# Kernel optimization log

Hardware: AMD Instinct MI355X
Metric: run time of the kernel (lower is better)

## Reference

```python
import jax, jax.numpy as jnp
import numpy as np
from jax import lax

NEG = jnp.float32(-1e30)  # log-domain 'zero'
BLANK = 0


def setup_inputs() -> dict:
    T, N, C, S = 512, 512, 80, 128
    k0, k1, k2, k3 = jax.random.split(jax.random.key(0), 4)
    logits = jax.random.normal(k0, (T, N, C), dtype=jnp.float32)
    log_probs = jax.nn.log_softmax(logits, axis=-1)  # CTCLoss expects log-probs
    targets = jax.random.randint(k1, (N, S), 1, C).astype(jnp.int32)  # labels in [1, C-1], blank=0 excluded
    input_lengths = jax.random.randint(k2, (N,), T // 2, T + 1).astype(jnp.int32)
    target_lengths = jax.random.randint(k3, (N,), S // 2, S + 1).astype(jnp.int32)
    return {"log_probs": log_probs, "targets": targets,
            "input_lengths": input_lengths, "target_lengths": target_lengths}


def _ctc_loss(log_probs, targets, input_lengths, target_lengths):
    # log_probs: (T, N, C) log-probabilities; targets: (N, S) labels (no blanks)
    T, N, C = log_probs.shape
    S = targets.shape[1]
    L = 2 * S + 1  # extended label length: blank-interleaved

    # extended targets: [blank, y1, blank, y2, ..., yS, blank]  -> (N, L)
    ext = jnp.zeros((N, L), jnp.int32).at[:, 1::2].set(targets)
    # skip transition (s-2 -> s) allowed only if ext[s] != ext[s-2]
    # (blank positions have ext[s]==ext[s-2]==blank, so this also forbids blank skips)
    skip_ok = jnp.pad(ext[:, 2:] != ext[:, :-2], ((0, 0), (2, 0)), constant_values=False)

    # emission log-probs on the lattice: (T, N, L)
    emit = jnp.take_along_axis(log_probs, jnp.broadcast_to(ext[None], (T, N, L)), axis=2)

    # alpha at t=0: only lattice positions 0 (blank) and 1 (first label) reachable
    alpha0 = jnp.full((N, L), NEG).at[:, 0].set(emit[0, :, 0]).at[:, 1].set(emit[0, :, 1])

    def step(alpha, xs):
        em, t = xs  # em: (N, L)
        a1 = jnp.pad(alpha[:, :-1], ((0, 0), (1, 0)), constant_values=NEG)
        a2 = jnp.where(skip_ok,
                       jnp.pad(alpha[:, :-2], ((0, 0), (2, 0)), constant_values=NEG), NEG)
        m = jnp.maximum(alpha, jnp.maximum(a1, a2))
        lse = m + jnp.log(jnp.exp(alpha - m) + jnp.exp(a1 - m) + jnp.exp(a2 - m))
        new = lse + em
        # freeze alpha for finished sequences (t >= input_length)
        alpha_new = jnp.where((t < input_lengths)[:, None], new, alpha)
        return alpha_new, None

    alpha_T, _ = lax.scan(step, alpha0, (emit[1:], jnp.arange(1, T, dtype=jnp.int32)))

    # final states: last blank (2*tl) and last label (2*tl - 1)
    i1 = (2 * target_lengths)[:, None]
    v1 = jnp.take_along_axis(alpha_T, i1, axis=1)[:, 0]
    v2 = jnp.take_along_axis(alpha_T, i1 - 1, axis=1)[:, 0]
    m = jnp.maximum(v1, v2)
    loss = -(m + jnp.log(jnp.exp(v1 - m) + jnp.exp(v2 - m)))
    # zero_infinity=True: infeasible alignments -> 0 loss
    loss = jnp.where(jnp.isfinite(loss) & (loss < 1e10), loss, 0.0)
    return loss  # (N,) reduction='none'


def reference(log_probs, targets, input_lengths, target_lengths):
    return _ctc_loss(log_probs, targets, input_lengths, target_lengths)
```

## Files before the change

### kernel.cpp

```cpp
#include <hip/hip_runtime.h>


#define NEGC  (-1.0e30f)
#define LOG2E 1.4426950408889634f
#define LN2   0.6931471805599453f

constexpr int T_ = 512;
constexpr int C_ = 80;
constexpr int S_ = 128;
constexpr int U_ = 8;
constexpr int WROW = 520;

__device__ __forceinline__ float exp2a(float x) { return __builtin_amdgcn_exp2f(x); }
__device__ __forceinline__ float log2a(float x) { return __builtin_amdgcn_logf(x); }

template <int CTRL>
__device__ __forceinline__ float dppf(float old_, float src) {
    return __int_as_float(__builtin_amdgcn_update_dpp(
        __float_as_int(old_), __float_as_int(src), CTRL, 0xF, 0xF, false));
}

__device__ __forceinline__ int wave_max_bits(float m) {
    m = fmaxf(m, dppf<0x111>(m, m));
    m = fmaxf(m, dppf<0x112>(m, m));
    m = fmaxf(m, dppf<0x114>(m, m));
    m = fmaxf(m, dppf<0x118>(m, m));
    m = fmaxf(m, dppf<0x142>(m, m));
    m = fmaxf(m, dppf<0x143>(m, m));
    return __builtin_amdgcn_readlane(__float_as_int(m), 63);
}

__device__ __forceinline__ float lse2(float x, float y) {
    float m = fmaxf(x, y);
    return m + log2a(1.0f + exp2a(-fabsf(x - y)));
}
__device__ __forceinline__ float lse3(float x, float y, float z) {
    float m = fmaxf(x, fmaxf(y, z));
    return m + log2a(exp2a(x - m) + exp2a(y - m) + exp2a(z - m));
}

__global__ __launch_bounds__(64, 1) void ctc_half(
    const float* __restrict__ lp, const int* __restrict__ tgt,
    const int* __restrict__ ilen, const int* __restrict__ tlen,
    float* __restrict__ ws, int N)
{
    const int b   = blockIdx.x;
    const int n   = b >> 1;
    const int dir = b & 1;
    const int l   = threadIdx.x;

    float* ga = ws + (size_t)n * WROW;
    float* gg = ga + 260;

    const int* tn = tgt + n * S_;
    const int ext1 = tn[2 * l];
    const int ext3 = tn[2 * l + 1];
    const int prev = (l > 0) ? tn[2 * l - 1] : 0;
    const bool skip1 = (l > 0) && (ext1 != prev);
    const bool skip3 = (ext3 != ext1);
    const bool skb3  = (l < 63) && (tn[2 * l + 2] != ext3);

    int len = ilen[n];
    len = len < 1 ? 1 : (len > T_ ? T_ : len);
    const int mid = len >> 1;

    const size_t rstride = (size_t)N * C_;
    const float* lpn = lp + (size_t)n * C_;
    const float* pB = lpn;
    const float* p1 = lpn + ext1;
    const float* p3 = lpn + ext3;

    float rb[U_], r1[U_], r3[U_];

    if (dir == 0) {
        const int last = mid - 1 > 0 ? mid - 1 : 0;
        #pragma unroll
        for (int u = 0; u < U_; ++u) {
            const int r = u + 1;
            const int rc = r < mid ? r : last;
            const size_t o = (size_t)rc * rstride;
            rb[r & 7] = pB[o]; r1[r & 7] = p1[o]; r3[r & 7] = p3[o];
        }
        float p0_ = 0.f, p1_ = 0.f, p2_ = 0.f, p3_ = 0.f, p4_ = 0.f;
        int   E = -60;
        if (l == 0) {
            p0_ = exp2a(pB[0] * LOG2E + 60.0f);
            p1_ = exp2a(p1[0] * LOG2E + 60.0f);
        }
        float PbC = exp2a(rb[1] * LOG2E);
        float P1C = exp2a(r1[1] * LOG2E);
        float P3C = exp2a(r3[1] * LOG2E);
        for (int tb = 1; tb < mid; tb += U_) {
            #pragma unroll
            for (int u = 0; u < U_; ++u) {
                const int t = tb + u;
                const int slot = (1 + u) & 7;
                const int rr = t + U_;
                const int rc = rr < mid ? rr : last;
                const size_t o = (size_t)rc * rstride;
                const float nrb = pB[o], nr1 = p1[o], nr3 = p3[o];
                const int ns = (2 + u) & 7;
                const float PbN = exp2a(rb[ns] * LOG2E);
                const float P1N = exp2a(r1[ns] * LOG2E);
                const float P3N = exp2a(r3[ns] * LOG2E);
                if (t < mid) {
                    const float sm1 = dppf<0x138>(0.0f, p3_);
                    const float i0 = p0_ + sm1;
                    const float i1 = p1_ + p0_ + (skip1 ? sm1 : 0.f);
                    const float i2 = p2_ + p1_;
                    const float i3 = p3_ + p2_ + (skip3 ? p1_ : 0.f);
                    const float i4 = p4_ + p3_;
                    p0_ = i0 * PbC; p1_ = i1 * P1C; p2_ = i2 * PbC;
                    p3_ = i3 * P3C; p4_ = i4 * PbC;
                }
                PbC = PbN; P1C = P1N; P3C = P3N;
                rb[slot] = nrb; r1[slot] = nr1; r3[slot] = nr3;
            }
            const int mi = wave_max_bits(
                fmaxf(fmaxf(fmaxf(p0_, p1_), fmaxf(p2_, p3_)), p4_));
            const int e = (mi > 0) ? (((mi >> 23) & 255) - 187) : 0;
            E += e;
            p0_ = ldexpf(p0_, -e); p1_ = ldexpf(p1_, -e); p2_ = ldexpf(p2_, -e);
            p3_ = ldexpf(p3_, -e); p4_ = ldexpf(p4_, -e);
        }
        const float fE = (float)E;
        ga[4 * l + 0] = (p0_ > 0.f) ? fmaxf(log2a(p0_) + fE, NEGC) : NEGC;
        ga[4 * l + 1] = (p1_ > 0.f) ? fmaxf(log2a(p1_) + fE, NEGC) : NEGC;
        ga[4 * l + 2] = (p2_ > 0.f) ? fmaxf(log2a(p2_) + fE, NEGC) : NEGC;
        ga[4 * l + 3] = (p3_ > 0.f) ? fmaxf(log2a(p3_) + fE, NEGC) : NEGC;
        if (l == 63) ga[256] = (p4_ > 0.f) ? fmaxf(log2a(p4_) + fE, NEGC) : NEGC;
    } else {
        const int fe = len - 1;
        #pragma unroll
        for (int u = 0; u < U_; ++u) {
            int rc = fe - 1 - u; if (rc < 0) rc = 0;
            const size_t o = (size_t)rc * rstride;
            rb[u] = pB[o]; r1[u] = p1[o]; r3[u] = p3[o];
        }
        const int tl = tlen[n];
        const int sA = 2 * tl, sB = 2 * tl - 1;
        float g0_, g1_, g2_, g3_, g4_;
        int E = -60;
        {
            const size_t o = (size_t)fe * rstride;
            const float ebi = pB[o] * LOG2E + 60.0f;
            const float e1i = p1[o] * LOG2E + 60.0f;
            const float e3i = p3[o] * LOG2E + 60.0f;
            const int s0 = 4 * l;
            g0_ = (s0     == sA)                 ? exp2a(ebi) : 0.f;
            g1_ = (s0 + 1 == sA || s0 + 1 == sB) ? exp2a(e1i) : 0.f;
            g2_ = (s0 + 2 == sA)                 ? exp2a(ebi) : 0.f;
            g3_ = (s0 + 3 == sA || s0 + 3 == sB) ? exp2a(e3i) : 0.f;
            g4_ = (l == 63 && 256 == sA)         ? exp2a(ebi) : 0.f;
        }
        float PbC = exp2a(rb[0] * LOG2E);
        float P1C = exp2a(r1[0] * LOG2E);
        float P3C = exp2a(r3[0] * LOG2E);
        for (int tb = fe - 1; tb >= mid; tb -= U_) {
            #pragma unroll
            for (int u = 0; u < U_; ++u) {
                const int t = tb - u;
                const int slot = u;
                int rc = t - U_; if (rc < 0) rc = 0;
                const size_t o = (size_t)rc * rstride;
                const float nrb = pB[o], nr1 = p1[o], nr3 = p3[o];
                const int ns = (u + 1) & 7;
                const float PbN = exp2a(rb[ns] * LOG2E);
                const float P1N = exp2a(r1[ns] * LOG2E);
                const float P3N = exp2a(r3[ns] * LOG2E);
                if (t >= mid) {
                    const float x0 = dppf<0x130>(g4_, g0_);
                    const float x1 = dppf<0x130>(0.f, g1_);
                    const float i0 = g0_ + g1_;
                    const float i1 = g1_ + g2_ + (skip3 ? g3_ : 0.f);
                    const float i2 = g2_ + g3_;
                    const float i3 = g3_ + x0 + (skb3 ? x1 : 0.f);
                    g0_ = i0 * PbC; g1_ = i1 * P1C; g2_ = i2 * PbC;
                    g3_ = i3 * P3C; g4_ = g4_ * PbC;
                }
                PbC = PbN; P1C = P1N; P3C = P3N;
                rb[slot] = nrb; r1[slot] = nr1; r3[slot] = nr3;
            }
            const int mi = wave_max_bits(
                fmaxf(fmaxf(fmaxf(g0_, g1_), fmaxf(g2_, g3_)), g4_));
            const int e = (mi > 0) ? (((mi >> 23) & 255) - 187) : 0;
            E += e;
            g0_ = ldexpf(g0_, -e); g1_ = ldexpf(g1_, -e); g2_ = ldexpf(g2_, -e);
            g3_ = ldexpf(g3_, -e); g4_ = ldexpf(g4_, -e);
        }
        const float fE = (float)E;
        gg[4 * l + 0] = (g0_ > 0.f) ? fmaxf(log2a(g0_) + fE, NEGC) : NEGC;
        gg[4 * l + 1] = (g1_ > 0.f) ? fmaxf(log2a(g1_) + fE, NEGC) : NEGC;
        gg[4 * l + 2] = (g2_ > 0.f) ? fmaxf(log2a(g2_) + fE, NEGC) : NEGC;
        gg[4 * l + 3] = (g3_ > 0.f) ? fmaxf(log2a(g3_) + fE, NEGC) : NEGC;
        if (l == 63) gg[256] = (g4_ > 0.f) ? fmaxf(log2a(g4_) + fE, NEGC) : NEGC;
    }
}

__global__ __launch_bounds__(64) void ctc_comb(
    const float* __restrict__ ws, const int* __restrict__ tgt,
    const int* __restrict__ ilen, const int* __restrict__ tlen,
    float* __restrict__ out, int N)
{
    const int n = blockIdx.x;
    const int l = threadIdx.x;
    const float* ga = ws + (size_t)n * WROW;
    const float* gg = ga + 260;

    int len = ilen[n];
    len = len < 1 ? 1 : (len > T_ ? T_ : len);
    const int tl = tlen[n];

    if (len == 1) {
        if (l == 0) {
            const float v1 = ga[2 * tl];
            const float v2 = (2 * tl >= 1) ? ga[2 * tl - 1] : NEGC;
            float loss = -lse2(v1, v2) * LN2;
            if (!(loss < 1e10f) || !isfinite(loss)) loss = 0.0f;
            out[n] = loss;
        }
        return;
    }

    const int* tn = tgt + n * S_;
    const int ext1 = tn[2 * l];
    const int ext3 = tn[2 * l + 1];
    const int prev = (l > 0) ? tn[2 * l - 1] : 0;
    const bool skip1 = (l > 0) && (ext1 != prev);
    const bool skip3 = (ext3 != ext1);

    const int s0 = 4 * l;
    const float Am1 = (l > 0) ? ga[s0 - 1] : NEGC;
    const float A0 = ga[s0], A1 = ga[s0 + 1], A2 = ga[s0 + 2], A3 = ga[s0 + 3];
    const float v0 = lse2(A0, Am1)                    + gg[s0];
    const float v1 = lse3(A1, A0, skip1 ? Am1 : NEGC) + gg[s0 + 1];
    const float v2 = lse2(A2, A1)                     + gg[s0 + 2];
    const float v3 = lse3(A3, A2, skip3 ? A1 : NEGC)  + gg[s0 + 3];
    const float v4 = (l == 63) ? (lse2(ga[256], A3) + gg[256]) : NEGC;

    float m = fmaxf(fmaxf(v0, v1), fmaxf(fmaxf(v2, v3), v4));
    float ssum = exp2a(v0 - m) + exp2a(v1 - m) + exp2a(v2 - m)
               + exp2a(v3 - m) + exp2a(v4 - m);
    float M = m;
    #pragma unroll
    for (int d = 1; d < 64; d <<= 1) M = fmaxf(M, __shfl_xor(M, d));
    float r = ssum * exp2a(m - M);
    #pragma unroll
    for (int d = 1; d < 64; d <<= 1) r += __shfl_xor(r, d);
    if (l == 0) {
        float loss = -LN2 * (M + log2a(r));
        if (!(loss < 1e10f) || !isfinite(loss)) loss = 0.0f;
        out[n] = loss;
    }
}

__global__ __launch_bounds__(128) void ctc_fused(
    const float* __restrict__ lp, const int* __restrict__ tgt,
    const int* __restrict__ ilen, const int* __restrict__ tlen,
    float* __restrict__ out, int N)
{
    const int n    = blockIdx.x;
    const int wave = threadIdx.x >> 6;
    const int l    = threadIdx.x & 63;

    __shared__ float ga[2 * S_ + 1];
    __shared__ float gg[2 * S_ + 1];

    const int* tn = tgt + n * S_;
    const int ext1 = tn[2 * l];
    const int ext3 = tn[2 * l + 1];
    const int prev = (l > 0) ? tn[2 * l - 1] : 0;
    const bool skip1 = (l > 0) && (ext1 != prev);
    const bool skip3 = (ext3 != ext1);
    const bool skb1 = (tn[2 * l + 1] != tn[2 * l]);
    const bool skb3 = (l < 63) && (tn[2 * l + 2] != tn[2 * l + 1]);

    int len = ilen[n];
    len = len < 1 ? 1 : (len > T_ ? T_ : len);
    const int mid = len >> 1;

    const size_t rstride = (size_t)N * C_;
    const float* lpn = lp + (size_t)n * C_;
    const float* pB = lpn;
    const float* p1 = lpn + ext1;
    const float* p3 = lpn + ext3;

    float rb[U_], r1[U_], r3[U_];

    if (wave == 0) {
        const int last = mid - 1 > 0 ? mid - 1 : 0;
        #pragma unroll
        for (int u = 0; u < U_; ++u) {
            const int r = u + 1;
            const int rc = r < mid ? r : last;
            const size_t o = (size_t)rc * rstride;
            rb[r & 7] = pB[o]; r1[r & 7] = p1[o]; r3[r & 7] = p3[o];
        }
        float a0 = NEGC, a1 = NEGC, a2 = NEGC, a3 = NEGC, a4 = NEGC;
        {
            const float i0 = pB[0] * LOG2E;
            const float i1 = p1[0] * LOG2E;
            if (l == 0) { a0 = i0; a1 = i1; }
        }
        for (int tb = 1; tb < mid; tb += U_) {
            #pragma unroll
            for (int u = 0; u < U_; ++u) {
                const int t = tb + u;
                const int slot = (1 + u) & 7;
                const float eb = rb[slot] * LOG2E;
                const float e1 = r1[slot] * LOG2E;
                const float e3 = r3[slot] * LOG2E;
                const int rr = t + U_;
                const int rc = rr < mid ? rr : last;
                const size_t o = (size_t)rc * rstride;
                const float nrb = pB[o], nr1 = p1[o], nr3 = p3[o];
                if (t < mid) {
                    const float sm1 = dppf<0x138>(NEGC, a3);
                    const float z1 = skip1 ? sm1 : NEGC;
                    const float z3 = skip3 ? a1  : NEGC;
                    const float n0 = lse2(a0, sm1)    + eb;
                    const float n1 = lse3(a1, a0, z1) + e1;
                    const float n2 = lse2(a2, a1)     + eb;
                    const float n3 = lse3(a3, a2, z3) + e3;
                    const float n4 = lse2(a4, a3)     + eb;
                    a0 = n0; a1 = n1; a2 = n2; a3 = n3; a4 = n4;
                }
                rb[slot] = nrb; r1[slot] = nr1; r3[slot] = nr3;
            }
        }
        ga[4 * l + 0] = a0; ga[4 * l + 1] = a1;
        ga[4 * l + 2] = a2; ga[4 * l + 3] = a3;
        if (l == 63) ga[256] = a4;
    } else {
        const int fe = len - 1;
        #pragma unroll
        for (int u = 0; u < U_; ++u) {
            int rc = fe - 1 - u; if (rc < 0) rc = 0;
            const size_t o = (size_t)rc * rstride;
            rb[u] = pB[o]; r1[u] = p1[o]; r3[u] = p3[o];
        }
        const int tl = tlen[n];
        const int sA = 2 * tl, sB = 2 * tl - 1;
        float g0, g1, g2, g3, g4;
        {
            const size_t o = (size_t)fe * rstride;
            const float ebi = pB[o] * LOG2E;
            const float e1i = p1[o] * LOG2E;
            const float e3i = p3[o] * LOG2E;
            const int s0 = 4 * l;
            g0 = (s0     == sA)                 ? ebi : NEGC;
            g1 = (s0 + 1 == sA || s0 + 1 == sB) ? e1i : NEGC;
            g2 = (s0 + 2 == sA)                 ? ebi : NEGC;
            g3 = (s0 + 3 == sA || s0 + 3 == sB) ? e3i : NEGC;
            g4 = (l == 63 && 256 == sA)         ? ebi : NEGC;
        }
        for (int tb = fe - 1; tb >= mid; tb -= U_) {
            #pragma unroll
            for (int u = 0; u < U_; ++u) {
                const int t = tb - u;
                const int slot = ((fe - 1 - tb) + u) & 7;
                const float eb = rb[slot] * LOG2E;
                const float e1 = r1[slot] * LOG2E;
                const float e3 = r3[slot] * LOG2E;
                int rc = t - U_; if (rc < 0) rc = 0;
                const size_t o = (size_t)rc * rstride;
                const float nrb = pB[o], nr1 = p1[o], nr3 = p3[o];
                if (t >= mid) {
                    const float nx0 = dppf<0x130>(g4,   g0);
                    const float nx1 = dppf<0x130>(NEGC, g1);
                    const float z1 = skb1 ? g3  : NEGC;
                    const float z3 = skb3 ? nx1 : NEGC;
                    const float n0 = lse2(g0, g1)      + eb;
                    const float n1 = lse3(g1, g2, z1)  + e1;
                    const float n2 = lse2(g2, g3)      + eb;
                    const float n3 = lse3(g3, nx0, z3) + e3;
                    const float n4 = g4 + eb;
                    g0 = n0; g1 = n1; g2 = n2; g3 = n3; g4 = n4;
                }
                rb[slot] = nrb; r1[slot] = nr1; r3[slot] = nr3;
            }
        }
        gg[4 * l + 0] = g0; gg[4 * l + 1] = g1;
        gg[4 * l + 2] = g2; gg[4 * l + 3] = g3;
        if (l == 63) gg[256] = g4;
    }

    __syncthreads();

    if (wave == 0) {
        const int tl = tlen[n];
        if (len == 1) {
            if (l == 0) {
                const float v1 = ga[2 * tl];
                const float v2 = (2 * tl >= 1) ? ga[2 * tl - 1] : NEGC;
                float loss = -lse2(v1, v2) * LN2;
                if (!(loss < 1e10f) || !isfinite(loss)) loss = 0.0f;
                out[n] = loss;
            }
            return;
        }
        const int s0 = 4 * l;
        const float Am1 = (l > 0) ? ga[s0 - 1] : NEGC;
        const float A0 = ga[s0], A1 = ga[s0 + 1], A2 = ga[s0 + 2], A3 = ga[s0 + 3];
        const float v0 = lse2(A0, Am1)                    + gg[s0];
        const float v1 = lse3(A1, A0, skip1 ? Am1 : NEGC) + gg[s0 + 1];
        const float v2 = lse2(A2, A1)                     + gg[s0 + 2];
        const float v3 = lse3(A3, A2, skip3 ? A1 : NEGC)  + gg[s0 + 3];
        const float v4 = (l == 63) ? (lse2(ga[256], A3) + gg[256]) : NEGC;

        float m = fmaxf(fmaxf(v0, v1), fmaxf(fmaxf(v2, v3), v4));
        float ssum = exp2a(v0 - m) + exp2a(v1 - m) + exp2a(v2 - m)
                   + exp2a(v3 - m) + exp2a(v4 - m);
        float M = m;
        #pragma unroll
        for (int d = 1; d < 64; d <<= 1) M = fmaxf(M, __shfl_xor(M, d));
        float r = ssum * exp2a(m - M);
        #pragma unroll
        for (int d = 1; d < 64; d <<= 1) r += __shfl_xor(r, d);
        if (l == 0) {
            float loss = -LN2 * (M + log2a(r));
            if (!(loss < 1e10f) || !isfinite(loss)) loss = 0.0f;
            out[n] = loss;
        }
    }
}

extern "C" void kernel_launch(void* const* d_in, const int* in_sizes, int n_in,
                              void* d_out, int out_size, void* d_ws, size_t ws_size,
                              hipStream_t stream) {
    const float* lp  = (const float*)d_in[0];
    const int*   tg  = (const int*)  d_in[1];
    const int*   il  = (const int*)  d_in[2];
    const int*   tl  = (const int*)  d_in[3];
    float*       out = (float*)d_out;
    const int N = in_sizes[2];
    const size_t need = (size_t)N * WROW * sizeof(float);
    if (ws_size >= need) {
        ctc_half<<<2 * N, 64, 0, stream>>>(lp, tg, il, tl, (float*)d_ws, N);
        ctc_comb<<<N, 64, 0, stream>>>((const float*)d_ws, tg, il, tl, out, N);
    } else {
        ctc_fused<<<N, 128, 0, stream>>>(lp, tg, il, tl, out, N);
    }
}
```

Before: 147.9 us.

## Stage full log-prob rows in LDS with coalesced double-buffered prefetch

Each wave now loads whole 80-class rows for 8 timesteps at a time with coalesced loads (10 per lane), pre-scales them by log2e and writes them to a double-buffered shared-memory ring. The recurrence then gathers its three emissions per step from LDS instead of issuing three scattered global loads per step. Loads are issued 16 steps ahead and the loop is restructured into two 8-step halves with renormalisation between them. This trades more global bytes (full rows rather than three values) and LDS traffic for fewer uncoalesced, latency-bound gathers on the serial critical path. There is no LDS barrier, which is acceptable only because the block is a single wave.

```diff
diff --git a/kernel.cpp b/kernel.cpp
--- a/kernel.cpp
+++ b/kernel.cpp
@@ -49,6 +49,8 @@
     const int dir = b & 1;
     const int l   = threadIdx.x;
 
+    __shared__ float lds[1280];
+
     float* ga = ws + (size_t)n * WROW;
     float* gg = ga + 260;
 
@@ -64,64 +66,100 @@
     len = len < 1 ? 1 : (len > T_ ? T_ : len);
     const int mid = len >> 1;
 
-    const size_t rstride = (size_t)N * C_;
+    const int irst = N * C_;
     const float* lpn = lp + (size_t)n * C_;
-    const float* pB = lpn;
-    const float* p1 = lpn + ext1;
-    const float* p3 = lpn + ext3;
-
-    float rb[U_], r1[U_], r3[U_];
+
+    int dkr[10], ckk[10];
+    #pragma unroll
+    for (int k = 0; k < 10; ++k) {
+        const unsigned flat = (unsigned)l + 64u * k;
+        const unsigned dk = flat / 80u;
+        ckk[k] = (int)(flat - 80u * dk);
+        dkr[k] = (int)dk * irst;
+    }
+
+    float VA[10], VB[10];
+
+#define SISSUE_F(FB, V) do {                                                   \
+    const int s_ = (FB) * irst;                                                \
+    _Pragma("unroll")                                                          \
+    for (int k = 0; k < 10; ++k)                                               \
+        V[k] = lpn[(unsigned)(s_ + dkr[k] + ckk[k])];                          \
+} while (0)
+
+#define SISSUE_B(FB, V) do {                                                   \
+    const int s_ = (FB) * irst;                                                \
+    _Pragma("unroll")                                                          \
+    for (int k = 0; k < 10; ++k) {                                             \
+        int v_ = s_ - dkr[k]; v_ = v_ < 0 ? 0 : v_;                            \
+        V[k] = lpn[(unsigned)(v_ + ckk[k])];                                   \
+    }                                                                          \
+} while (0)
+
+#define SWRITE(H, V) do {                                                      \
+    _Pragma("unroll")                                                          \
+    for (int k = 0; k < 10; ++k)                                               \
+        lds[(H) * 640 + l + 64 * k] = V[k] * LOG2E;                            \
+} while (0)
+
+#define RENORM(S0, S1, S2, S3, S4) do {                                        \
+    const int mi_ = wave_max_bits(                                             \
+        fmaxf(fmaxf(fmaxf(S0, S1), fmaxf(S2, S3)), S4));                       \
+    const int e_ = (mi_ > 0) ? (((mi_ >> 23) & 255) - 187) : 0;                \
+    E += e_;                                                                   \
+    S0 = ldexpf(S0, -e_); S1 = ldexpf(S1, -e_); S2 = ldexpf(S2, -e_);          \
+    S3 = ldexpf(S3, -e_); S4 = ldexpf(S4, -e_);                                \
+} while (0)
 
     if (dir == 0) {
-        const int last = mid - 1 > 0 ? mid - 1 : 0;
-        #pragma unroll
-        for (int u = 0; u < U_; ++u) {
-            const int r = u + 1;
-            const int rc = r < mid ? r : last;
-            const size_t o = (size_t)rc * rstride;
-            rb[r & 7] = pB[o]; r1[r & 7] = p1[o]; r3[r & 7] = p3[o];
-        }
+        SISSUE_F(1, VA);  SWRITE(0, VA);
+        SISSUE_F(9, VB);  SWRITE(1, VB);
+        SISSUE_F(17, VA);
+
         float p0_ = 0.f, p1_ = 0.f, p2_ = 0.f, p3_ = 0.f, p4_ = 0.f;
         int   E = -60;
         if (l == 0) {
-            p0_ = exp2a(pB[0] * LOG2E + 60.0f);
-            p1_ = exp2a(p1[0] * LOG2E + 60.0f);
-        }
-        float PbC = exp2a(rb[1] * LOG2E);
-        float P1C = exp2a(r1[1] * LOG2E);
-        float P3C = exp2a(r3[1] * LOG2E);
-        for (int tb = 1; tb < mid; tb += U_) {
-            #pragma unroll
-            for (int u = 0; u < U_; ++u) {
-                const int t = tb + u;
-                const int slot = (1 + u) & 7;
-                const int rr = t + U_;
-                const int rc = rr < mid ? rr : last;
-                const size_t o = (size_t)rc * rstride;
-                const float nrb = pB[o], nr1 = p1[o], nr3 = p3[o];
-                const int ns = (2 + u) & 7;
-                const float PbN = exp2a(rb[ns] * LOG2E);
-                const float P1N = exp2a(r1[ns] * LOG2E);
-                const float P3N = exp2a(r3[ns] * LOG2E);
-                if (t < mid) {
-                    const float sm1 = dppf<0x138>(0.0f, p3_);
-                    const float i0 = p0_ + sm1;
-                    const float i1 = p1_ + p0_ + (skip1 ? sm1 : 0.f);
-                    const float i2 = p2_ + p1_;
-                    const float i3 = p3_ + p2_ + (skip3 ? p1_ : 0.f);
-                    const float i4 = p4_ + p3_;
-                    p0_ = i0 * PbC; p1_ = i1 * P1C; p2_ = i2 * PbC;
-                    p3_ = i3 * P3C; p4_ = i4 * PbC;
-                }
-                PbC = PbN; P1C = P1N; P3C = P3N;
-                rb[slot] = nrb; r1[slot] = nr1; r3[slot] = nr3;
-            }
-            const int mi = wave_max_bits(
-                fmaxf(fmaxf(fmaxf(p0_, p1_), fmaxf(p2_, p3_)), p4_));
-            const int e = (mi > 0) ? (((mi >> 23) & 255) - 187) : 0;
-            E += e;
-            p0_ = ldexpf(p0_, -e); p1_ = ldexpf(p1_, -e); p2_ = ldexpf(p2_, -e);
-            p3_ = ldexpf(p3_, -e); p4_ = ldexpf(p4_, -e);
+            p0_ = exp2a(lpn[0] * LOG2E + 60.0f);
+            p1_ = exp2a(lpn[ext1] * LOG2E + 60.0f);
+        }
+        float PbC = exp2a(lds[0]);
+        float P1C = exp2a(lds[ext1]);
+        float P3C = exp2a(lds[ext3]);
+        float rbN = lds[80], r1N = lds[80 + ext1], r3N = lds[80 + ext3];
+
+#define FWD_STEP(T_EXPR) do {                                                  \
+    const int t_ = (T_EXPR);                                                   \
+    const int idx2_ = t_ + 1;                        \
+    const int ofs2_ = ((idx2_ >> 3) & 1) * 640 + (idx2_ & 7) * 80;             \
+    const float rb2_ = lds[ofs2_];                                             \
+    const float r12_ = lds[ofs2_ + ext1];                                      \
+    const float r32_ = lds[ofs2_ + ext3];                                      \
+    const float PbN_ = exp2a(rbN), P1N_ = exp2a(r1N), P3N_ = exp2a(r3N);       \
+    if (t_ < mid) {                                                            \
+        const float sm1_ = dppf<0x138>(0.0f, p3_);          \
+        const float i0_ = p0_ + sm1_;                                          \
+        const float i1_ = p1_ + p0_ + (skip1 ? sm1_ : 0.f);                    \
+        const float i2_ = p2_ + p1_;                                           \
+        const float i3_ = p3_ + p2_ + (skip3 ? p1_ : 0.f);                     \
+        const float i4_ = p4_ + p3_;                                           \
+        p0_ = i0_ * PbC; p1_ = i1_ * P1C; p2_ = i2_ * PbC;                     \
+        p3_ = i3_ * P3C; p4_ = i4_ * PbC;                                      \
+    }                                                                          \
+    PbC = PbN_; P1C = P1N_; P3C = P3N_;                                        \
+    rbN = rb2_; r1N = r12_; r3N = r32_;                                        \
+} while (0)
+
+        for (int tb = 1; tb < mid; tb += 16) {
+            #pragma unroll
+            for (int u = 0; u < 8; ++u) FWD_STEP(tb + u);
+            RENORM(p0_, p1_, p2_, p3_, p4_);
+            SWRITE(0, VA);
+            SISSUE_F(tb + 24, VB);
+            #pragma unroll
+            for (int u = 8; u < 16; ++u) FWD_STEP(tb + u);
+            RENORM(p0_, p1_, p2_, p3_, p4_);
+            SWRITE(1, VB);
+            SISSUE_F(tb + 32, VA);
         }
         const float fE = (float)E;
         ga[4 * l + 0] = (p0_ > 0.f) ? fmaxf(log2a(p0_) + fE, NEGC) : NEGC;
@@ -131,21 +169,19 @@
         if (l == 63) ga[256] = (p4_ > 0.f) ? fmaxf(log2a(p4_) + fE, NEGC) : NEGC;
     } else {
         const int fe = len - 1;
-        #pragma unroll
-        for (int u = 0; u < U_; ++u) {
-            int rc = fe - 1 - u; if (rc < 0) rc = 0;
-            const size_t o = (size_t)rc * rstride;
-            rb[u] = pB[o]; r1[u] = p1[o]; r3[u] = p3[o];
-        }
+        SISSUE_B(fe - 1, VA);  SWRITE(0, VA);
+        SISSUE_B(fe - 9, VB);  SWRITE(1, VB);
+        SISSUE_B(fe - 17, VA);
+
         const int tl = tlen[n];
         const int sA = 2 * tl, sB = 2 * tl - 1;
         float g0_, g1_, g2_, g3_, g4_;
         int E = -60;
         {
-            const size_t o = (size_t)fe * rstride;
-            const float ebi = pB[o] * LOG2E + 60.0f;
-            const float e1i = p1[o] * LOG2E + 60.0f;
-            const float e3i = p3[o] * LOG2E + 60.0f;
+            const unsigned feo = (unsigned)(fe * irst);
+            const float ebi = lpn[feo] * LOG2E + 60.0f;
+            const float e1i = lpn[feo + ext1] * LOG2E + 60.0f;
+            const float e3i = lpn[feo + ext3] * LOG2E + 60.0f;
             const int s0 = 4 * l;
             g0_ = (s0     == sA)                 ? exp2a(ebi) : 0.f;
             g1_ = (s0 + 1 == sA || s0 + 1 == sB) ? exp2a(e1i) : 0.f;
@@ -153,40 +189,44 @@
             g3_ = (s0 + 3 == sA || s0 + 3 == sB) ? exp2a(e3i) : 0.f;
             g4_ = (l == 63 && 256 == sA)         ? exp2a(ebi) : 0.f;
         }
-        float PbC = exp2a(rb[0] * LOG2E);
-        float P1C = exp2a(r1[0] * LOG2E);
-        float P3C = exp2a(r3[0] * LOG2E);
-        for (int tb = fe - 1; tb >= mid; tb -= U_) {
-            #pragma unroll
-            for (int u = 0; u < U_; ++u) {
-                const int t = tb - u;
-                const int slot = u;
-                int rc = t - U_; if (rc < 0) rc = 0;
-                const size_t o = (size_t)rc * rstride;
-                const float nrb = pB[o], nr1 = p1[o], nr3 = p3[o];
-                const int ns = (u + 1) & 7;
-                const float PbN = exp2a(rb[ns] * LOG2E);
-                const float P1N = exp2a(r1[ns] * LOG2E);
-                const float P3N = exp2a(r3[ns] * LOG2E);
-                if (t >= mid) {
-                    const float x0 = dppf<0x130>(g4_, g0_);
-                    const float x1 = dppf<0x130>(0.f, g1_);
-                    const float i0 = g0_ + g1_;
-                    const float i1 = g1_ + g2_ + (skip3 ? g3_ : 0.f);
-                    const float i2 = g2_ + g3_;
-                    const float i3 = g3_ + x0 + (skb3 ? x1 : 0.f);
-                    g0_ = i0 * PbC; g1_ = i1 * P1C; g2_ = i2 * PbC;
-                    g3_ = i3 * P3C; g4_ = g4_ * PbC;
-                }
-                PbC = PbN; P1C = P1N; P3C = P3N;
-                rb[slot] = nrb; r1[slot] = nr1; r3[slot] = nr3;
-            }
-            const int mi = wave_max_bits(
-                fmaxf(fmaxf(fmaxf(g0_, g1_), fmaxf(g2_, g3_)), g4_));
-            const int e = (mi > 0) ? (((mi >> 23) & 255) - 187) : 0;
-            E += e;
-            g0_ = ldexpf(g0_, -e); g1_ = ldexpf(g1_, -e); g2_ = ldexpf(g2_, -e);
-            g3_ = ldexpf(g3_, -e); g4_ = ldexpf(g4_, -e);
+        float PbC = exp2a(lds[0]);
+        float P1C = exp2a(lds[ext1]);
+        float P3C = exp2a(lds[ext3]);
+        float rbN = lds[80], r1N = lds[80 + ext1], r3N = lds[80 + ext3];
+
+#define BWD_STEP(T_EXPR) do {                                                  \
+    const int t_ = (T_EXPR);                                                   \
+    const int idx2_ = fe + 1 - t_;                   \
+    const int ofs2_ = ((idx2_ >> 3) & 1) * 640 + (idx2_ & 7) * 80;             \
+    const float rb2_ = lds[ofs2_];                                             \
+    const float r12_ = lds[ofs2_ + ext1];                                      \
+    const float r32_ = lds[ofs2_ + ext3];                                      \
+    const float PbN_ = exp2a(rbN), P1N_ = exp2a(r1N), P3N_ = exp2a(r3N);       \
+    if (t_ >= mid) {                                                           \
+        const float x0_ = dppf<0x130>(g4_, g0_);      \
+        const float x1_ = dppf<0x130>(0.f, g1_);      \
+        const float i0_ = g0_ + g1_;                                           \
+        const float i1_ = g1_ + g2_ + (skip3 ? g3_ : 0.f);                     \
+        const float i2_ = g2_ + g3_;                                           \
+        const float i3_ = g3_ + x0_ + (skb3 ? x1_ : 0.f);                      \
+        g0_ = i0_ * PbC; g1_ = i1_ * P1C; g2_ = i2_ * PbC;                     \
+        g3_ = i3_ * P3C; g4_ = g4_ * PbC;                                      \
+    }                                                                          \
+    PbC = PbN_; P1C = P1N_; P3C = P3N_;                                        \
+    rbN = rb2_; r1N = r12_; r3N = r32_;                                        \
+} while (0)
+
+        for (int tb = fe - 1; tb >= mid; tb -= 16) {
+            #pragma unroll
+            for (int u = 0; u < 8; ++u) BWD_STEP(tb - u);
+            RENORM(g0_, g1_, g2_, g3_, g4_);
+            SWRITE(0, VA);
+            SISSUE_B(tb - 24, VB);
+            #pragma unroll
+            for (int u = 8; u < 16; ++u) BWD_STEP(tb - u);
+            RENORM(g0_, g1_, g2_, g3_, g4_);
+            SWRITE(1, VB);
+            SISSUE_B(tb - 32, VA);
         }
         const float fE = (float)E;
         gg[4 * l + 0] = (g0_ > 0.f) ? fmaxf(log2a(g0_) + fE, NEGC) : NEGC;
@@ -195,6 +235,12 @@
         gg[4 * l + 3] = (g3_ > 0.f) ? fmaxf(log2a(g3_) + fE, NEGC) : NEGC;
         if (l == 63) gg[256] = (g4_ > 0.f) ? fmaxf(log2a(g4_) + fE, NEGC) : NEGC;
     }
+#undef FWD_STEP
+#undef BWD_STEP
+#undef SISSUE_F
+#undef SISSUE_B
+#undef SWRITE
+#undef RENORM
 }
 
 __global__ __launch_bounds__(64) void ctc_comb(
```

Measured after the change: 131.9 us. -10.8%, faster.
